# Kernel tuning notes

Measured on AMD Instinct MI355X. Metric: run time of the kernel, lower is better.

Reference implementation:

```python
import jax, jax.numpy as jnp
import numpy as np

V, E, P, T = 65536, 4096, 4096, 512
SENT = 1e9    # finite sentinel for masked min/max (keeps grads NaN-free)
BIG = 1e30    # 'never the minimum' sentinel for invalid points


def setup_inputs() -> dict:
    key = jax.random.key(0)
    k1, k2, k3, k4 = jax.random.split(key, 4)
    verts = jax.random.uniform(k1, (V, 3), dtype=jnp.float32)
    e0 = jax.random.randint(k2, (E,), 0, V - 1)
    edges = jnp.stack([e0, e0 + 1], axis=1)          # distinct endpoints
    listAll = jax.random.randint(k3, (P,), 0, V)
    TableR = jax.random.uniform(k4, (T, 7), dtype=jnp.float32)
    return {"verts": verts, "TableR": TableR, "edges": edges,
            "listAll": listAll, "epoch": 1, "pth": 0}


def _mouth_loss(verts, TableR, edges, listAll):
    v2 = verts[:, :2]                 # deleteaxeZ
    p = v2[listAll]                   # [P,2] query points
    px, py = p[:, 0], p[:, 1]
    ev = v2[edges]                    # [E,2,2]
    x0, y0 = ev[:, 0, 0], ev[:, 0, 1]
    x1, y1 = ev[:, 1, 0], ev[:, 1, 1]
    a = (y0 - y1) / (x0 - x1)         # edge line y = a*x + b (order-invariant)
    b = y0 - a * x0

    # getexpose: first edge with min_x < px < max_x (falls back to last edge)
    xmn, xmx = jnp.minimum(x0, x1), jnp.maximum(x0, x1)
    condA = (px[:, None] > xmn[None, :]) & (px[:, None] < xmx[None, :])  # [P,E]
    idx = jnp.where(condA.any(1), jnp.argmax(condA, axis=1), E - 1)
    exposeY = a[idx] * px + b[idx]
    L1 = jnp.sqrt((py - exposeY) ** 2)        # expose shares x with p -> dx=0
    cy = (py + exposeY) * 0.5                 # centre1 = midpoint (cx == px)
    cx = px

    # getpoints: intersections of horizontal ray y=cy with every edge
    ymn, ymx = jnp.minimum(y0, y1), jnp.maximum(y0, y1)
    condB = (cy[:, None] > ymn[None, :]) & (cy[:, None] < ymx[None, :])  # [P,E]
    xi = (cy[:, None] - b[None, :]) / a[None, :]                          # [P,E]
    n = condB.sum(1)
    xall_mx = jnp.max(jnp.where(condB, xi, -SENT), axis=1)
    xall_mn = jnp.min(jnp.where(condB, xi, SENT), axis=1)
    spu = condB & (xi >= cx[:, None])   # right side (incl. equal, per original)
    inf_ = condB & (xi < cx[:, None])   # left side
    xs = jnp.min(jnp.where(spu, xi, SENT), axis=1)    # minimum of spu
    xinf = jnp.max(jnp.where(inf_, xi, -SENT), axis=1)  # maximum of inf
    has_both = spu.any(1) & inf_.any(1)
    valid = (n == 2) | ((n > 2) & has_both)
    dx = jnp.where(n == 2, xall_mx - xall_mn, xs - xinf)
    L2 = jnp.sqrt(dx ** 2)                    # both points share y=cy
    d1 = jnp.sqrt((cy - 1.0) ** 2)            # dist([1, cy], Ref=(1,1))
    d2 = jnp.sqrt((px - 1.0) ** 2)            # dist([px, 1], Ref=(1,1))

    # al vs every table row (only columns 3..6 are used by the original)
    al = (jnp.abs(L1[:, None] - TableR[None, :, 3])
          + jnp.abs(L2[:, None] - TableR[None, :, 4])
          + jnp.abs(d1[:, None] - TableR[None, :, 5])
          + jnp.abs(d2[:, None] - TableR[None, :, 6]))          # [P,T]
    pm = jnp.min(al, axis=1)                  # per-point best table match
    # `error` is never reset in the original -> running min across points
    m = jnp.where(valid, pm, BIG)
    run = jax.lax.cummin(m, axis=0)
    return jnp.sum(jnp.where(valid, run, 0.0))


def reference(verts, TableR, edges, listAll, epoch, pth):
    # epoch/pth only gate .obj file dumping in the original; no math effect.
    return _mouth_loss(verts, TableR, edges, listAll)
```

## Files before the change

### kernel.cpp

```cpp
#include <hip/hip_runtime.h>
#include <math.h>

#define NV 65536
#define NE 4096
#define NP 4096
#define NT 512
#define SENTF 1000000000.0f
#define BIGF 1e30f

__device__ __forceinline__ float waveMinF(float v) {
    #pragma unroll
    for (int o = 32; o; o >>= 1) v = fminf(v, __shfl_xor(v, o, 64));
    return v;
}
__device__ __forceinline__ float waveMaxF(float v) {
    #pragma unroll
    for (int o = 32; o; o >>= 1) v = fmaxf(v, __shfl_xor(v, o, 64));
    return v;
}
__device__ __forceinline__ int waveSumI(int v) {
    #pragma unroll
    for (int o = 32; o; o >>= 1) v += __shfl_xor(v, o, 64);
    return v;
}
__device__ __forceinline__ int waveMinI(int v) {
    #pragma unroll
    for (int o = 32; o; o >>= 1) v = min(v, __shfl_xor(v, o, 64));
    return v;
}

__global__ void prep_kernel(const float* __restrict__ verts,
                            const int*   __restrict__ edges,
                            const float* __restrict__ tab,
                            float*  __restrict__ ea,  float*  __restrict__ eb,
                            float2* __restrict__ pk2, float4* __restrict__ pk4,
                            float4* __restrict__ tb4) {
    int e = blockIdx.x * blockDim.x + threadIdx.x;
    if (e < NT) {
        const float* r = tab + 7 * e;
        tb4[e] = make_float4(r[3], r[4], r[5], r[6]);
    }
    if (e >= NE) return;
    int i0 = edges[2 * e + 0];
    int i1 = edges[2 * e + 1];
    float x0 = verts[3 * i0 + 0], y0 = verts[3 * i0 + 1];
    float x1 = verts[3 * i1 + 0], y1 = verts[3 * i1 + 1];
    float a = (y0 - y1) / (x0 - x1);
    float b = y0 - a * x0;
    ea[e] = a; eb[e] = b;
    pk2[e] = make_float2(fminf(x0, x1), fmaxf(x0, x1));
    pk4[e] = make_float4(fminf(y0, y1), fmaxf(y0, y1), 1.0f / a, b);
}

__global__ __launch_bounds__(1024) void point_kernel(
        const float*  __restrict__ verts,
        const int*    __restrict__ listAll,
        const float*  __restrict__ ea,  const float*  __restrict__ eb,
        const float2* __restrict__ pk2, const float4* __restrict__ pk4,
        const float4* __restrict__ tb4,
        float* __restrict__ mOut, int* __restrict__ validOut) {
    __shared__ float4 sE[NE];

    int tid  = threadIdx.x;
    int lane = tid & 63;
    int wid  = tid >> 6;
    int p    = blockIdx.x * 16 + wid;

    float4 r0 = pk4[tid];
    float4 r1 = pk4[1024 + tid];
    float4 r2 = pk4[2048 + tid];
    float4 r3 = pk4[3072 + tid];

    int   vi = listAll[p];
    float px = verts[3 * vi + 0];
    float py = verts[3 * vi + 1];

    int minIdx = NE;
    for (int it = 0; it < NE / 64; ++it) {
        int e = it * 64 + lane;
        float2 q = pk2[e];
        bool hit = (px > q.x) && (px < q.y);
        if (hit) minIdx = e;
        if (__any(hit)) break;
    }
    minIdx = waveMinI(minIdx);
    int idx = (minIdx >= NE) ? (NE - 1) : minIdx;

    float exposeY = ea[idx] * px + eb[idx];
    float L1 = fabsf(py - exposeY);
    float cy = 0.5f * (py + exposeY);
    float cx = px;

    sE[tid]        = r0;
    sE[1024 + tid] = r1;
    sE[2048 + tid] = r2;
    sE[3072 + tid] = r3;
    __syncthreads();

    int   n = 0, hasS = 0, hasI = 0;
    float xallmx = -SENTF, xallmn = SENTF;
    float xs = SENTF, xinf = -SENTF;
    #pragma unroll 8
    for (int it = 0; it < NE / 64; ++it) {
        float4 q = sE[it * 64 + lane];
        bool  c  = (cy > q.x) && (cy < q.y);
        float xi = (cy - q.w) * q.z;
        n += c ? 1 : 0;
        xallmx = fmaxf(xallmx, c ? xi : -SENTF);
        xallmn = fminf(xallmn, c ? xi :  SENTF);
        bool sp  = c && (xi >= cx);
        bool in_ = c && (xi <  cx);
        xs   = fminf(xs,   sp  ? xi :  SENTF);
        xinf = fmaxf(xinf, in_ ? xi : -SENTF);
        hasS |= sp ? 1 : 0;
        hasI |= in_ ? 1 : 0;
    }
    int packed = n | (hasS << 16) | (hasI << 24);
    packed = waveSumI(packed);
    xallmx = waveMaxF(xallmx);
    xallmn = waveMinF(xallmn);
    xs     = waveMinF(xs);
    xinf   = waveMaxF(xinf);
    n    = packed & 0xFFFF;
    hasS = (packed >> 16) & 0xFF;
    hasI = (packed >> 24) & 0xFF;

    bool valid = (n == 2) || ((n > 2) && (hasS > 0) && (hasI > 0));
    float dx = (n == 2) ? (xallmx - xallmn) : (xs - xinf);
    float L2 = fabsf(dx);
    float d1 = fabsf(cy - 1.0f);
    float d2 = fabsf(px - 1.0f);

    float pm = INFINITY;
    #pragma unroll
    for (int k = 0; k < NT / 64; ++k) {
        float4 r = tb4[k * 64 + lane];
        float al = fabsf(L1 - r.x) + fabsf(L2 - r.y) +
                   fabsf(d1 - r.z) + fabsf(d2 - r.w);
        pm = fminf(pm, al);
    }
    pm = waveMinF(pm);

    if (lane == 0) {
        mOut[p]     = valid ? pm : BIGF;
        validOut[p] = valid ? 1 : 0;
    }
}

__global__ __launch_bounds__(1024) void scan_kernel(const float* __restrict__ m,
                                                    const int*   __restrict__ valid,
                                                    float* __restrict__ out) {
    __shared__ float wAgg[16];
    __shared__ float wSum[16];
    int t = threadIdx.x;
    int lane = t & 63, wid = t >> 6;

    float v[4]; int vl[4];
    #pragma unroll
    for (int j = 0; j < 4; j++) { v[j] = m[4 * t + j]; vl[j] = valid[4 * t + j]; }
    float cmin = fminf(fminf(v[0], v[1]), fminf(v[2], v[3]));

    float inc = cmin;
    #pragma unroll
    for (int o = 1; o < 64; o <<= 1) {
        float u = __shfl_up(inc, o, 64);
        if (lane >= o) inc = fminf(inc, u);
    }
    if (lane == 63) wAgg[wid] = inc;
    __syncthreads();

    float wavePrefix = INFINITY;
    for (int i = 0; i < wid; i++) wavePrefix = fminf(wavePrefix, wAgg[i]);
    float excl = __shfl_up(inc, 1, 64);
    if (lane == 0) excl = INFINITY;
    float run = fminf(wavePrefix, excl);

    float sum = 0.0f;
    #pragma unroll
    for (int j = 0; j < 4; j++) {
        run = fminf(run, v[j]);
        if (vl[j]) sum += run;
    }
    #pragma unroll
    for (int o = 32; o; o >>= 1) sum += __shfl_xor(sum, o, 64);
    if (lane == 0) wSum[wid] = sum;
    __syncthreads();
    if (t == 0) {
        float s = 0.0f;
        for (int i = 0; i < 16; i++) s += wSum[i];
        out[0] = s;
    }
}

extern "C" void kernel_launch(void* const* d_in, const int* in_sizes, int n_in,
                              void* d_out, int out_size, void* d_ws, size_t ws_size,
                              hipStream_t stream) {
    const float* verts   = (const float*)d_in[0];
    const float* tab     = (const float*)d_in[1];
    const int*   edges   = (const int*)d_in[2];
    const int*   listAll = (const int*)d_in[3];

    char* ws = (char*)d_ws;
    float4* pk4 = (float4*)ws;                     ws += NE * sizeof(float4);
    float4* tb4 = (float4*)ws;                     ws += NT * sizeof(float4);
    float2* pk2 = (float2*)ws;                     ws += NE * sizeof(float2);
    float*  ea  = (float*)ws;                      ws += NE * sizeof(float);
    float*  eb  = (float*)ws;                      ws += NE * sizeof(float);
    float*  mArr= (float*)ws;                      ws += NP * sizeof(float);
    int*    vArr= (int*)ws;

    prep_kernel<<<(NE + 255) / 256, 256, 0, stream>>>(verts, edges, tab, ea, eb, pk2, pk4, tb4);
    point_kernel<<<NP / 16, 1024, 0, stream>>>(verts, listAll, ea, eb, pk2, pk4, tb4, mArr, vArr);
    scan_kernel<<<1, 1024, 0, stream>>>(mArr, vArr, (float*)d_out);
}
```

Measured before the change: 28.94 us.

## Split edge scan across waves, 4 lanes per point, block-level reduction

The edge-intersection scan is repartitioned. Previously each wave scanned all 4096 edges for one point. Now each wave handles a 256-edge slice for all 16 points of the block, with 4 lanes per point. Partial min/max/count values are reduced with two shuffle steps and then combined across waves through shared memory. This shortens the per-wave reduction and spreads the work differently, at the cost of two extra block-wide syncs and a serial 16-way shared-memory combine.

```diff
diff --git a/kernel.cpp b/kernel.cpp
--- a/kernel.cpp
+++ b/kernel.cpp
@@ -5,22 +5,14 @@
 #define NE 4096
 #define NP 4096
 #define NT 512
+#define NPB 16
+#define EW  256
 #define SENTF 1000000000.0f
 #define BIGF 1e30f
 
 __device__ __forceinline__ float waveMinF(float v) {
     #pragma unroll
     for (int o = 32; o; o >>= 1) v = fminf(v, __shfl_xor(v, o, 64));
-    return v;
-}
-__device__ __forceinline__ float waveMaxF(float v) {
-    #pragma unroll
-    for (int o = 32; o; o >>= 1) v = fmaxf(v, __shfl_xor(v, o, 64));
-    return v;
-}
-__device__ __forceinline__ int waveSumI(int v) {
-    #pragma unroll
-    for (int o = 32; o; o >>= 1) v += __shfl_xor(v, o, 64);
     return v;
 }
 __device__ __forceinline__ int waveMinI(int v) {
@@ -58,38 +50,45 @@
         const float*  __restrict__ ea,  const float*  __restrict__ eb,
         const float2* __restrict__ pk2, const float4* __restrict__ pk4,
         const float4* __restrict__ tb4,
-        float* __restrict__ mOut, int* __restrict__ validOut) {
+        float* __restrict__ mOut, int* __restrict__ vOut) {
     __shared__ float4 sE[NE];
-
-    int tid  = threadIdx.x;
-    int lane = tid & 63;
-    int wid  = tid >> 6;
-    int p    = blockIdx.x * 16 + wid;
+    __shared__ float  sW[16][NPB][5];
+    __shared__ float  sF[NPB][5];
+    __shared__ float  sCY[NPB], sPX[NPB], sL1[NPB], sL2[NPB];
+    __shared__ int    sVal[NPB];
+
+    const int tid  = threadIdx.x;
+    const int lane = tid & 63;
+    const int w    = tid >> 6;
+    const int pBase = blockIdx.x * NPB;
 
     float4 r0 = pk4[tid];
     float4 r1 = pk4[1024 + tid];
     float4 r2 = pk4[2048 + tid];
     float4 r3 = pk4[3072 + tid];
 
-    int   vi = listAll[p];
-    float px = verts[3 * vi + 0];
-    float py = verts[3 * vi + 1];
-
-    int minIdx = NE;
-    for (int it = 0; it < NE / 64; ++it) {
-        int e = it * 64 + lane;
-        float2 q = pk2[e];
-        bool hit = (px > q.x) && (px < q.y);
-        if (hit) minIdx = e;
-        if (__any(hit)) break;
-    }
-    minIdx = waveMinI(minIdx);
-    int idx = (minIdx >= NE) ? (NE - 1) : minIdx;
-
-    float exposeY = ea[idx] * px + eb[idx];
-    float L1 = fabsf(py - exposeY);
-    float cy = 0.5f * (py + exposeY);
-    float cx = px;
+    {
+        int p  = pBase + w;
+        int vi = listAll[p];
+        float px = verts[3 * vi + 0];
+        float py = verts[3 * vi + 1];
+        int minIdx = NE;
+        for (int it = 0; it < NE / 64; ++it) {
+            int e = it * 64 + lane;
+            float2 q = pk2[e];
+            bool hit = (px > q.x) && (px < q.y);
+            if (hit) minIdx = e;
+            if (__any(hit)) break;
+        }
+        minIdx = waveMinI(minIdx);
+        int idx = (minIdx >= NE) ? (NE - 1) : minIdx;
+        float exposeY = ea[idx] * px + eb[idx];
+        if (lane == 0) {
+            sCY[w] = 0.5f * (py + exposeY);
+            sL1[w] = fabsf(py - exposeY);
+            sPX[w] = px;
+        }
+    }
 
     sE[tid]        = r0;
     sE[1024 + tid] = r1;
@@ -97,53 +96,108 @@
     sE[3072 + tid] = r3;
     __syncthreads();
 
-    int   n = 0, hasS = 0, hasI = 0;
+    const int   pl  = lane >> 2;
+    const int   s   = lane & 3;
+    const float cyl = sCY[pl];
+    const float cxl = sPX[pl];
+
+    int   nAcc = 0, hasS = 0, hasI = 0;
     float xallmx = -SENTF, xallmn = SENTF;
     float xs = SENTF, xinf = -SENTF;
     #pragma unroll 8
-    for (int it = 0; it < NE / 64; ++it) {
-        float4 q = sE[it * 64 + lane];
-        bool  c  = (cy > q.x) && (cy < q.y);
-        float xi = (cy - q.w) * q.z;
-        n += c ? 1 : 0;
+    for (int k = 0; k < EW / 4; ++k) {
+        float4 q4 = sE[w * EW + k * 4 + s];
+        bool  c  = (cyl > q4.x) && (cyl < q4.y);
+        float xi = (cyl - q4.w) * q4.z;
+        nAcc += c ? 1 : 0;
         xallmx = fmaxf(xallmx, c ? xi : -SENTF);
         xallmn = fminf(xallmn, c ? xi :  SENTF);
-        bool sp  = c && (xi >= cx);
-        bool in_ = c && (xi <  cx);
+        bool sp  = c && (xi >= cxl);
+        bool in_ = c && (xi <  cxl);
         xs   = fminf(xs,   sp  ? xi :  SENTF);
         xinf = fmaxf(xinf, in_ ? xi : -SENTF);
         hasS |= sp ? 1 : 0;
         hasI |= in_ ? 1 : 0;
     }
-    int packed = n | (hasS << 16) | (hasI << 24);
-    packed = waveSumI(packed);
-    xallmx = waveMaxF(xallmx);
-    xallmn = waveMinF(xallmn);
-    xs     = waveMinF(xs);
-    xinf   = waveMaxF(xinf);
-    n    = packed & 0xFFFF;
-    hasS = (packed >> 16) & 0xFF;
-    hasI = (packed >> 24) & 0xFF;
-
-    bool valid = (n == 2) || ((n > 2) && (hasS > 0) && (hasI > 0));
-    float dx = (n == 2) ? (xallmx - xallmn) : (xs - xinf);
-    float L2 = fabsf(dx);
-    float d1 = fabsf(cy - 1.0f);
-    float d2 = fabsf(px - 1.0f);
-
-    float pm = INFINITY;
-    #pragma unroll
-    for (int k = 0; k < NT / 64; ++k) {
-        float4 r = tb4[k * 64 + lane];
-        float al = fabsf(L1 - r.x) + fabsf(L2 - r.y) +
-                   fabsf(d1 - r.z) + fabsf(d2 - r.w);
-        pm = fminf(pm, al);
-    }
-    pm = waveMinF(pm);
-
-    if (lane == 0) {
-        mOut[p]     = valid ? pm : BIGF;
-        validOut[p] = valid ? 1 : 0;
+
+    int packed = nAcc | (hasS << 16) | (hasI << 24);
+    #pragma unroll
+    for (int o = 1; o <= 2; o <<= 1) {
+        xallmx = fmaxf(xallmx, __shfl_xor(xallmx, o, 64));
+        xallmn = fminf(xallmn, __shfl_xor(xallmn, o, 64));
+        xs     = fminf(xs,     __shfl_xor(xs,     o, 64));
+        xinf   = fmaxf(xinf,   __shfl_xor(xinf,   o, 64));
+        packed += __shfl_xor(packed, o, 64);
+    }
+    if (s == 0) {
+        sW[w][pl][0] = xallmx;
+        sW[w][pl][1] = xallmn;
+        sW[w][pl][2] = xs;
+        sW[w][pl][3] = xinf;
+        sW[w][pl][4] = __int_as_float(packed);
+    }
+    __syncthreads();
+
+    if (tid < 80) {
+        int pp = tid & 15, st = tid >> 4;
+        if (st == 0) {
+            float a0 = sW[0][pp][0];
+            #pragma unroll
+            for (int ww = 1; ww < 16; ++ww) a0 = fmaxf(a0, sW[ww][pp][0]);
+            sF[pp][0] = a0;
+        } else if (st == 1) {
+            float a0 = sW[0][pp][1];
+            #pragma unroll
+            for (int ww = 1; ww < 16; ++ww) a0 = fminf(a0, sW[ww][pp][1]);
+            sF[pp][1] = a0;
+        } else if (st == 2) {
+            float a0 = sW[0][pp][2];
+            #pragma unroll
+            for (int ww = 1; ww < 16; ++ww) a0 = fminf(a0, sW[ww][pp][2]);
+            sF[pp][2] = a0;
+        } else if (st == 3) {
+            float a0 = sW[0][pp][3];
+            #pragma unroll
+            for (int ww = 1; ww < 16; ++ww) a0 = fmaxf(a0, sW[ww][pp][3]);
+            sF[pp][3] = a0;
+        } else {
+            int a0 = __float_as_int(sW[0][pp][4]);
+            #pragma unroll
+            for (int ww = 1; ww < 16; ++ww) a0 += __float_as_int(sW[ww][pp][4]);
+            sF[pp][4] = __int_as_float(a0);
+        }
+    }
+    __syncthreads();
+
+    if (tid < NPB) {
+        int pn = __float_as_int(sF[tid][4]);
+        int n  = pn & 0xFFFF;
+        int hS = (pn >> 16) & 0xFF;
+        int hI = (pn >> 24) & 0xFF;
+        bool valid = (n == 2) || ((n > 2) && (hS > 0) && (hI > 0));
+        float dx = (n == 2) ? (sF[tid][0] - sF[tid][1]) : (sF[tid][2] - sF[tid][3]);
+        sL2[tid]  = fabsf(dx);
+        sVal[tid] = valid ? 1 : 0;
+    }
+    __syncthreads();
+
+    {
+        float L1v = sL1[w], L2v = sL2[w];
+        float d1  = fabsf(sCY[w] - 1.0f);
+        float d2  = fabsf(sPX[w] - 1.0f);
+        float pm = INFINITY;
+        #pragma unroll
+        for (int kk = 0; kk < NT / 64; ++kk) {
+            float4 r = tb4[kk * 64 + lane];
+            float al = fabsf(L1v - r.x) + fabsf(L2v - r.y) +
+                       fabsf(d1 - r.z) + fabsf(d2 - r.w);
+            pm = fminf(pm, al);
+        }
+        pm = waveMinF(pm);
+        if (lane == 0) {
+            mOut[pBase + w] = sVal[w] ? pm : BIGF;
+            vOut[pBase + w] = sVal[w];
+        }
     }
 }
 
@@ -201,15 +255,18 @@
     const int*   listAll = (const int*)d_in[3];
 
     char* ws = (char*)d_ws;
-    float4* pk4 = (float4*)ws;                     ws += NE * sizeof(float4);
-    float4* tb4 = (float4*)ws;                     ws += NT * sizeof(float4);
-    float2* pk2 = (float2*)ws;                     ws += NE * sizeof(float2);
-    float*  ea  = (float*)ws;                      ws += NE * sizeof(float);
-    float*  eb  = (float*)ws;                      ws += NE * sizeof(float);
-    float*  mArr= (float*)ws;                      ws += NP * sizeof(float);
+    float4* pk4 = (float4*)ws;                    ws += NE * sizeof(float4);
+    float4* tb4 = (float4*)ws;                    ws += NT * sizeof(float4);
+    float2* pk2 = (float2*)ws;                    ws += NE * sizeof(float2);
+    float*  ea  = (float*)ws;                     ws += NE * sizeof(float);
+    float*  eb  = (float*)ws;                     ws += NE * sizeof(float);
+    float*  mArr= (float*)ws;                     ws += NP * sizeof(float);
     int*    vArr= (int*)ws;
 
-    prep_kernel<<<(NE + 255) / 256, 256, 0, stream>>>(verts, edges, tab, ea, eb, pk2, pk4, tb4);
-    point_kernel<<<NP / 16, 1024, 0, stream>>>(verts, listAll, ea, eb, pk2, pk4, tb4, mArr, vArr);
+    prep_kernel<<<(NE + 255) / 256, 256, 0, stream>>>(verts, edges, tab,
+                                                      ea, eb, pk2, pk4, tb4);
+    point_kernel<<<NP / NPB, 1024, 0, stream>>>(verts, listAll,
+                                                ea, eb, pk2, pk4, tb4,
+                                                mArr, vArr);
     scan_kernel<<<1, 1024, 0, stream>>>(mArr, vArr, (float*)d_out);
 }
```

After: 29.37 us. About the same (+1.5%).
